# Kernel optimization log

Measured on AMD Instinct MI355X. Metric: run time of the kernel, lower is better.

## Reference

```python
import jax, jax.numpy as jnp
import numpy as np

HID = 1024
HEADS = 16
DH = HID // HEADS
SCALE = DH ** -0.5
L, B = 2048, 2


def setup_inputs() -> dict:
    key = jax.random.key(0)
    ks = jax.random.split(key, 16)
    inp = {
        "query": jax.random.normal(ks[0], (L, B, HID), jnp.float32),
        "key": jax.random.normal(ks[1], (L, B, HID), jnp.float32),
        "value": jax.random.normal(ks[2], (L, B, HID), jnp.float32),
        "mask": jax.random.randint(ks[3], (B, L), 0, 2).astype(bool),
    }
    # xavier-uniform linear weights (torch Linear stores [out, in]; y = x @ W.T + b)
    lim = (6.0 / (HID + HID)) ** 0.5
    for i, name in enumerate(["wq", "wk", "wv", "wfc"]):
        inp[name] = jax.random.uniform(ks[4 + i], (HID, HID), jnp.float32, -lim, lim)
    inp["bq"] = jnp.zeros((HID,), jnp.float32)
    inp["bk"] = jnp.zeros((HID,), jnp.float32)
    inp["bv"] = jnp.zeros((HID,), jnp.float32)
    inp["bfc"] = jnp.zeros((HID,), jnp.float32)
    inp["tao"] = jnp.full((HEADS,), 10.0, jnp.float32)
    return inp


def reference(query, key, value, mask, wq, bq, wk, bk, wv, bv, wfc, bfc, tao):
    # inputs arrive [L, B, D]; module transposes to [B, L, D]
    q = jnp.swapaxes(query, 0, 1)
    k = jnp.swapaxes(key, 0, 1)
    v = jnp.swapaxes(value, 0, 1)
    bsz, length, _ = q.shape

    def heads(x, w, b):
        y = x @ w.T + b                      # [B, L, D]
        return y.reshape(bsz, length, HEADS, DH).transpose(0, 2, 1, 3)  # [B, H, L, d]

    Q = heads(q, wq, bq)
    K = heads(k, wk, bk)
    V = heads(v, wv, bv)

    qk = jnp.einsum("bhqd,bhkd->bhqk", Q, K) * SCALE  # [B, H, L, L]

    # gaussian positional bias: -|i-j|^2/2 * tao_h^-4
    idx = jnp.arange(length, dtype=jnp.float32)
    dist = -0.5 * (idx[:, None] - idx[None, :]) ** 2          # [L, L]
    qk = qk + dist[None, None, :, :] * (tao ** -4)[None, :, None, None]

    qk = jnp.where(mask[:, None, None, :], -jnp.inf, qk)
    attn = jax.nn.softmax(qk, axis=-1)  # dropout is identity in eval mode

    x = jnp.einsum("bhqk,bhkd->bhqd", attn, V)            # [B, H, L, d]
    x = x.transpose(0, 2, 1, 3).reshape(bsz, length, HID)  # [B, L, D]
    x = x @ wfc.T + bfc
    return jnp.swapaxes(x, 0, 1)  # [L, B, D]
```

## Files before the change

kernel.cpp:

```cpp
#include <hip/hip_runtime.h>

#define LQ   2048
#define BQ   2
#define HID  1024
#define NH   16
#define DH   64
#define SCALE 0.125f
#define L2E  1.44269504088896f
#define C1   0.18033688011f
#define EXPOFF 23.0831206542f
#define MASKNEG (-1024.0f)

using short8  = __attribute__((ext_vector_type(8))) short;
using ushort8 = __attribute__((ext_vector_type(8))) unsigned short;
using f32x4   = __attribute__((ext_vector_type(4))) float;
typedef unsigned short u16;
typedef __attribute__((ext_vector_type(2))) __bf16 bf16x2;

__device__ inline u16 f2bf(float x) {
    unsigned int u = __float_as_uint(x);
    u = (u + 0x7fffu + ((u >> 16) & 1u)) >> 16;
    return (u16)u;
}

#if defined(__has_builtin)
#if __has_builtin(__builtin_amdgcn_cvt_pk_bf16_f32)
#define HAVE_PKBF 1
#endif
#if __has_builtin(__builtin_amdgcn_exp2f)
#define HAVE_EXP2 1
#endif
#endif

__device__ inline unsigned int pkbf(float a, float b) {
#ifdef HAVE_PKBF
    bf16x2 r = __builtin_amdgcn_cvt_pk_bf16_f32(a, b);
    return __builtin_bit_cast(unsigned int, r);
#else
    return (unsigned int)f2bf(a) | ((unsigned int)f2bf(b) << 16);
#endif
}

__device__ inline float fexp2(float x) {
#ifdef HAVE_EXP2
    return __builtin_amdgcn_exp2f(x);
#else
    return exp2f(x);
#endif
}

__device__ inline void gl_lds16(const void* g, void* l) {
    __builtin_amdgcn_global_load_lds(
        (const __attribute__((address_space(1))) void*)g,
        (__attribute__((address_space(3))) void*)l, 16, 0, 0);
}

struct CastArgs {
    const float* s[7];
    u16* d[7];
    int n[7];
    const unsigned char* mraw;
    float* mout;
    int mn;
};

__global__ __launch_bounds__(256) void castw(CastArgs a) {
    const int y = blockIdx.y;
    const int t = threadIdx.x;
    if (y == 7) {
        if (blockIdx.x != 0) return;
        __shared__ int cnt;
        if (t == 0) cnt = 0;
        __syncthreads();
        int local = 0;
        for (int i = t; i < a.mn; i += 256)
            if ((i & 3) && a.mraw[i]) local++;
        atomicAdd(&cnt, local);
        __syncthreads();
        bool isInt32 = (cnt == 0);
        const int* mi = (const int*)a.mraw;
        for (int i = t; i < a.mn; i += 256) {
            const bool m = isInt32 ? (mi[i] != 0) : (a.mraw[i] != 0);
            a.mout[i] = m ? (MASKNEG - EXPOFF) : (-EXPOFF);
        }
        return;
    }
    const float* s = a.s[y];
    u16* d = a.d[y];
    const int n4 = a.n[y] >> 2;
    for (int i = blockIdx.x * 256 + t; i < n4; i += gridDim.x * 256) {
        float4 v = *(const float4*)(s + (size_t)i * 4);
        uint2 p;
        p.x = pkbf(v.x, v.y);
        p.y = pkbf(v.z, v.w);
        *(uint2*)(d + (size_t)i * 4) = p;
    }
}

struct QkvArgs {
    const u16* A[3];
    const u16* W[3];
    const float* bias[3];
    u16* out[3];
};

__global__ __launch_bounds__(256) void gemm_qkv(QkvArgs ga) {
    __shared__ u16 As[2][128][64];
    __shared__ u16 Bs[2][128][64];

    const int z = blockIdx.z;
    const u16* A = ga.A[z];
    const u16* W = ga.W[z];
    const float* bias = ga.bias[z];
    u16* outp = ga.out[z];

    const int t = threadIdx.x;
    const int m0 = blockIdx.x * 128;
    const int n0 = blockIdx.y * 128;
    const int lane = t & 63;
    const int lane15 = lane & 15;
    const int quad = lane >> 4;
    const int w = t >> 6;
    const int wm = (w >> 1) * 64;
    const int wn = (w & 1) * 64;

    const int lrow = lane >> 3;
    const int ch = (lane & 7) ^ ((lane >> 3) & 7);
    const u16* aS = A + (size_t)(m0 + 32 * w + lrow) * HID + 8 * ch;
    const u16* bS = W + (size_t)(n0 + 32 * w + lrow) * HID + 8 * ch;

    const int s0 = (quad ^ (lane15 & 7)) * 8;
    const int s1 = ((4 + quad) ^ (lane15 & 7)) * 8;

    f32x4 acc[4][4];
#pragma unroll
    for (int i = 0; i < 4; i++)
#pragma unroll
        for (int j = 0; j < 4; j++) acc[i][j] = (f32x4){0,0,0,0};

#pragma unroll
    for (int i = 0; i < 4; i++) {
        gl_lds16(aS + (size_t)(8 * i) * HID, &As[0][32 * w + 8 * i][0]);
        gl_lds16(bS + (size_t)(8 * i) * HID, &Bs[0][32 * w + 8 * i][0]);
    }
    __syncthreads();

    int p = 0;
    for (int k0 = 0; k0 < HID; k0 += 64) {
        short8 af0[4], af1[4], bf0[4], bf1[4];
#pragma unroll
        for (int i = 0; i < 4; i++) {
            const u16* ar = &As[p][wm + i * 16 + lane15][0];
            const u16* br = &Bs[p][wn + i * 16 + lane15][0];
            af0[i] = *(const short8*)(ar + s0);
            af1[i] = *(const short8*)(ar + s1);
            bf0[i] = *(const short8*)(br + s0);
            bf1[i] = *(const short8*)(br + s1);
        }
        if (k0 + 64 < HID) {
#pragma unroll
            for (int i = 0; i < 4; i++) {
                gl_lds16(aS + (size_t)(8 * i) * HID + (k0 + 64), &As[p ^ 1][32 * w + 8 * i][0]);
                gl_lds16(bS + (size_t)(8 * i) * HID + (k0 + 64), &Bs[p ^ 1][32 * w + 8 * i][0]);
            }
        }
#pragma unroll
        for (int mi = 0; mi < 4; mi++)
#pragma unroll
            for (int ni = 0; ni < 4; ni++) {
                acc[mi][ni] = __builtin_amdgcn_mfma_f32_16x16x32_bf16(af0[mi], bf0[ni], acc[mi][ni], 0, 0, 0);
                acc[mi][ni] = __builtin_amdgcn_mfma_f32_16x16x32_bf16(af1[mi], bf1[ni], acc[mi][ni], 0, 0, 0);
            }
        __syncthreads();
        p ^= 1;
    }

#pragma unroll
    for (int mi = 0; mi < 4; mi++) {
#pragma unroll
        for (int ni = 0; ni < 4; ni++) {
            const int n = n0 + wn + ni * 16 + lane15;
            const float bv = bias[n];
            const int h = n >> 6, d = n & 63;
#pragma unroll
            for (int r = 0; r < 4; r++) {
                const int m = m0 + wm + mi * 16 + quad * 4 + r;
                const float c = acc[mi][ni][r] + bv;
                const int b = m & 1, l = m >> 1;
                if (z < 2) {
                    outp[(((size_t)(b * NH + h)) * LQ + l) * DH + d] = f2bf(c);
                } else {
                    outp[(((size_t)(b * NH + h)) * DH + d) * LQ + l] = f2bf(c);
                }
            }
        }
    }
}

__global__ __launch_bounds__(256) void gemm_fc(const u16* __restrict__ A,
                                               const u16* __restrict__ W,
                                               const float* __restrict__ bias,
                                               float* __restrict__ outp) {
    __shared__ u16 As[2][128][64];
    __shared__ u16 Bs[2][64][64];

    const int t = threadIdx.x;
    const int m0 = blockIdx.x * 128;
    const int n0 = blockIdx.y * 64;
    const int lane = t & 63;
    const int lane15 = lane & 15;
    const int quad = lane >> 4;
    const int w = t >> 6;
    const int wm = (w >> 1) * 64;
    const int wn = (w & 1) * 32;

    const int lrow = lane >> 3;
    const int ch = (lane & 7) ^ ((lane >> 3) & 7);
    const u16* aS = A + (size_t)(m0 + 32 * w + lrow) * HID + 8 * ch;
    const u16* bS = W + (size_t)(n0 + 16 * w + lrow) * HID + 8 * ch;

    const int s0 = (quad ^ (lane15 & 7)) * 8;
    const int s1 = ((4 + quad) ^ (lane15 & 7)) * 8;

    f32x4 acc[4][2];
#pragma unroll
    for (int i = 0; i < 4; i++)
#pragma unroll
        for (int j = 0; j < 2; j++) acc[i][j] = (f32x4){0,0,0,0};

#pragma unroll
    for (int i = 0; i < 4; i++)
        gl_lds16(aS + (size_t)(8 * i) * HID, &As[0][32 * w + 8 * i][0]);
#pragma unroll
    for (int i = 0; i < 2; i++)
        gl_lds16(bS + (size_t)(8 * i) * HID, &Bs[0][16 * w + 8 * i][0]);
    __syncthreads();

    int p = 0;
    for (int k0 = 0; k0 < HID; k0 += 64) {
        short8 af0[4], af1[4], bf0[2], bf1[2];
#pragma unroll
        for (int i = 0; i < 4; i++) {
            const u16* ar = &As[p][wm + i * 16 + lane15][0];
            af0[i] = *(const short8*)(ar + s0);
            af1[i] = *(const short8*)(ar + s1);
        }
#pragma unroll
        for (int j = 0; j < 2; j++) {
            const u16* br = &Bs[p][wn + j * 16 + lane15][0];
            bf0[j] = *(const short8*)(br + s0);
            bf1[j] = *(const short8*)(br + s1);
        }
        if (k0 + 64 < HID) {
#pragma unroll
            for (int i = 0; i < 4; i++)
                gl_lds16(aS + (size_t)(8 * i) * HID + (k0 + 64), &As[p ^ 1][32 * w + 8 * i][0]);
#pragma unroll
            for (int i = 0; i < 2; i++)
                gl_lds16(bS + (size_t)(8 * i) * HID + (k0 + 64), &Bs[p ^ 1][16 * w + 8 * i][0]);
        }
#pragma unroll
        for (int mi = 0; mi < 4; mi++)
#pragma unroll
            for (int ni = 0; ni < 2; ni++) {
                acc[mi][ni] = __builtin_amdgcn_mfma_f32_16x16x32_bf16(af0[mi], bf0[ni], acc[mi][ni], 0, 0, 0);
                acc[mi][ni] = __builtin_amdgcn_mfma_f32_16x16x32_bf16(af1[mi], bf1[ni], acc[mi][ni], 0, 0, 0);
            }
        __syncthreads();
        p ^= 1;
    }

#pragma unroll
    for (int mi = 0; mi < 4; mi++) {
#pragma unroll
        for (int ni = 0; ni < 2; ni++) {
            const int n = n0 + wn + ni * 16 + lane15;
            const float bv = bias[n];
#pragma unroll
            for (int r = 0; r < 4; r++) {
                const int m = m0 + wm + mi * 16 + quad * 4 + r;
                outp[(size_t)m * HID + n] = acc[mi][ni][r] + bv;
            }
        }
    }
}

#define PSTR 72

__global__ __launch_bounds__(256, 3) void attn_kernel(const u16* __restrict__ Qg,
                                                      const u16* __restrict__ Kg,
                                                      const u16* __restrict__ Vtg,
                                                      const float* __restrict__ maskF,
                                                      const float* __restrict__ tao,
                                                      u16* __restrict__ Xa) {
    __shared__ u16 Ks[2][64][64];
    __shared__ u16 Vt[2][64][64];
    __shared__ u16 PT[64][PSTR];

    const int bh = blockIdx.x;
    const int q0 = blockIdx.y * 64;
    const int b = bh >> 4;
    const int h = bh & 15;
    const int t = threadIdx.x;
    const int w = t >> 6;
    const int lane = t & 63;
    const int lane15 = lane & 15;
    const int quad = lane >> 4;

    const u16* Kbase = Kg + (size_t)bh * LQ * DH;
    const u16* Vtbase = Vtg + (size_t)bh * DH * LQ;
    const float* mrow = maskF + b * LQ;

    const float tv = tao[h];
    const float t2 = tv * tv;
    const float nb = -0.5f / (t2 * t2);
    const float nb2 = nb * L2E;
    const float sqn = sqrtf(-nb2);
    const float R = sqrtf(-40.0f / nb2) + 1.0f;

    int c_lo = (int)floorf(((float)q0 - R) * (1.0f / 64.0f));
    int c_hi = (int)floorf(((float)(q0 + 63) + R) * (1.0f / 64.0f));
    if (c_lo < 0) c_lo = 0;
    if (c_hi > (LQ / 64 - 1)) c_hi = LQ / 64 - 1;
    if (c_hi < c_lo) c_hi = c_lo;

    const int lr = lane >> 3;
    const int sch = (lane & 7) ^ lr;
    const u16* kS0 = Kbase + (size_t)(16 * w + lr) * DH + 8 * sch;
    const u16* kS1 = Kbase + (size_t)(16 * w + 8 + lr) * DH + 8 * sch;
    const u16* vS0 = Vtbase + (size_t)(16 * w + lr) * LQ + 8 * sch;
    const u16* vS1 = Vtbase + (size_t)(16 * w + 8 + lr) * LQ + 8 * sch;

    const int qrow = q0 + w * 16 + lane15;
    short8 qB0, qB1;
    {
        const u16* qp_ = Qg + ((size_t)bh * LQ + qrow) * DH + quad * 8;
        qB0 = *(const short8*)(qp_);
        qB1 = *(const short8*)(qp_ + 32);
    }

    const int s0 = (quad ^ (lane15 & 7)) * 8;
    const int s1 = ((4 + quad) ^ (lane15 & 7)) * 8;

    float crs[16];
#pragma unroll
    for (int i = 0; i < 16; i++)
        crs[i] = (float)((i >> 2) * 16 + (i & 3)) * sqn;

    short8 ones;
#pragma unroll
    for (int i = 0; i < 8; i++) ones[i] = (short)0x3F80;

    f32x4 O[4];
#pragma unroll
    for (int mt = 0; mt < 4; mt++) O[mt] = (f32x4){0,0,0,0};
    f32x4 Lacc = (f32x4){0,0,0,0};

    const float eb0 = (float)(qrow - quad * 4);
    const int prow = w * 16 + lane15;

    gl_lds16(kS0 + (size_t)c_lo * (64 * DH), &Ks[0][16 * w][0]);
    gl_lds16(kS1 + (size_t)c_lo * (64 * DH), &Ks[0][16 * w + 8][0]);
    gl_lds16(vS0 + 64 * c_lo, &Vt[0][16 * w][0]);
    gl_lds16(vS1 + 64 * c_lo, &Vt[0][16 * w + 8][0]);
    __syncthreads();

    int p = 0;
    for (int c = c_lo; c <= c_hi; ++c) {
        float4 mv[4];
#pragma unroll
        for (int kt = 0; kt < 4; kt++)
            mv[kt] = *(const float4*)(mrow + 64 * c + kt * 16 + quad * 4);

        if (c < c_hi) {
            gl_lds16(kS0 + (size_t)(c + 1) * (64 * DH), &Ks[p ^ 1][16 * w][0]);
            gl_lds16(kS1 + (size_t)(c + 1) * (64 * DH), &Ks[p ^ 1][16 * w + 8][0]);
            gl_lds16(vS0 + 64 * (c + 1), &Vt[p ^ 1][16 * w][0]);
            gl_lds16(vS1 + 64 * (c + 1), &Vt[p ^ 1][16 * w + 8][0]);
        }

        f32x4 S[4];
#pragma unroll
        for (int kt = 0; kt < 4; kt++) {
            const u16* kr = &Ks[p][kt * 16 + lane15][0];
            const short8 ka = *(const short8*)(kr + s0);
            const short8 kb = *(const short8*)(kr + s1);
            S[kt] = __builtin_amdgcn_mfma_f32_16x16x32_bf16(ka, qB0, (f32x4){0,0,0,0}, 0, 0, 0);
            S[kt] = __builtin_amdgcn_mfma_f32_16x16x32_bf16(kb, qB1, S[kt], 0, 0, 0);
        }

        const float ebS = (eb0 - (float)(64 * c)) * sqn;
        float lacc_dummy;
        (void)lacc_dummy;
#pragma unroll
        for (int kt = 0; kt < 4; kt++) {
            float pr[4];
#pragma unroll
            for (int r = 0; r < 4; r++) {
                const float dp = ebS - crs[kt * 4 + r];
                const float tb = fmaf(-dp, dp, ((const float*)&mv[kt])[r]);
                pr[r] = fexp2(fmaf(S[kt][r], C1, tb));
            }
            uint2 pk2;
            pk2.x = pkbf(pr[0], pr[1]);
            pk2.y = pkbf(pr[2], pr[3]);
            *(uint2*)&PT[prow][kt * 16 + quad * 4] = pk2;
        }

        const short8 pB0 = *(const short8*)&PT[prow][quad * 8];
        const short8 pB1 = *(const short8*)&PT[prow][32 + quad * 8];
        Lacc = __builtin_amdgcn_mfma_f32_16x16x32_bf16(ones, pB0, Lacc, 0, 0, 0);
        Lacc = __builtin_amdgcn_mfma_f32_16x16x32_bf16(ones, pB1, Lacc, 0, 0, 0);
#pragma unroll
        for (int mt = 0; mt < 4; mt++) {
            const u16* vr = &Vt[p][mt * 16 + lane15][0];
            const short8 va = *(const short8*)(vr + s0);
            const short8 vb = *(const short8*)(vr + s1);
            O[mt] = __builtin_amdgcn_mfma_f32_16x16x32_bf16(va, pB0, O[mt], 0, 0, 0);
            O[mt] = __builtin_amdgcn_mfma_f32_16x16x32_bf16(vb, pB1, O[mt], 0, 0, 0);
        }

        __syncthreads();
        p ^= 1;
    }

    {
        const float inv = 1.0f / Lacc[0];
        u16* dst = Xa + ((size_t)qrow * BQ + b) * HID + h * DH;
#pragma unroll
        for (int mt = 0; mt < 4; mt++) {
            uint2 pk2;
            pk2.x = pkbf(O[mt][0] * inv, O[mt][1] * inv);
            pk2.y = pkbf(O[mt][2] * inv, O[mt][3] * inv);
            *(uint2*)(dst + mt * 16 + quad * 4) = pk2;
        }
    }
}

extern "C" void kernel_launch(void* const* d_in, const int* in_sizes, int n_in,
                              void* d_out, int out_size, void* d_ws, size_t ws_size,
                              hipStream_t stream) {
    const float* q    = (const float*)d_in[0];
    const float* k    = (const float*)d_in[1];
    const float* v    = (const float*)d_in[2];
    const void*  mask = d_in[3];
    const float* wq   = (const float*)d_in[4];
    const float* wk   = (const float*)d_in[5];
    const float* wv   = (const float*)d_in[6];
    const float* wfc  = (const float*)d_in[7];
    const float* bq   = (const float*)d_in[8];
    const float* bk   = (const float*)d_in[9];
    const float* bv   = (const float*)d_in[10];
    const float* bfc  = (const float*)d_in[11];
    const float* tao  = (const float*)d_in[12];

    const size_t NE = (size_t)LQ * BQ * HID;
    const size_t NW = (size_t)HID * HID;
    u16* base = (u16*)d_ws;
    u16* Qp    = base;
    u16* Kp    = base + NE;
    u16* Vtp   = base + 2 * NE;
    u16* Xa    = base + 3 * NE;
    u16* qbf   = base + 4 * NE;
    u16* kbf   = base + 5 * NE;
    u16* vbf   = base + 6 * NE;
    u16* wqbf  = base + 7 * NE;
    u16* wkbf  = wqbf + NW;
    u16* wvbf  = wkbf + NW;
    u16* wfcbf = wvbf + NW;
    float* maskF = (float*)(wfcbf + NW);

    CastArgs ca;
    ca.s[0] = q;   ca.d[0] = qbf;   ca.n[0] = (int)NE;
    ca.s[1] = k;   ca.d[1] = kbf;   ca.n[1] = (int)NE;
    ca.s[2] = v;   ca.d[2] = vbf;   ca.n[2] = (int)NE;
    ca.s[3] = wq;  ca.d[3] = wqbf;  ca.n[3] = (int)NW;
    ca.s[4] = wk;  ca.d[4] = wkbf;  ca.n[4] = (int)NW;
    ca.s[5] = wv;  ca.d[5] = wvbf;  ca.n[5] = (int)NW;
    ca.s[6] = wfc; ca.d[6] = wfcbf; ca.n[6] = (int)NW;
    ca.mraw = (const unsigned char*)mask;
    ca.mout = maskF;
    ca.mn = BQ * LQ;
    castw<<<dim3(256, 8), 256, 0, stream>>>(ca);

    QkvArgs ga;
    ga.A[0] = qbf;  ga.W[0] = wqbf;  ga.bias[0] = bq;  ga.out[0] = Qp;
    ga.A[1] = kbf;  ga.W[1] = wkbf;  ga.bias[1] = bk;  ga.out[1] = Kp;
    ga.A[2] = vbf;  ga.W[2] = wvbf;  ga.bias[2] = bv;  ga.out[2] = Vtp;
    gemm_qkv<<<dim3(32, 8, 3), 256, 0, stream>>>(ga);

    attn_kernel<<<dim3(32, 32), 256, 0, stream>>>(Qp, Kp, Vtp, maskF, tao, Xa);

    gemm_fc<<<dim3(32, 16), 256, 0, stream>>>(Xa, wfcbf, bfc, (float*)d_out);
}
```

Before: 236.5 us.

## Process 128 query rows per attention block to reuse K/V tiles twice

Each attention block now covers 128 query rows instead of 64, with every wave handling two 16-row query subtiles that share the same K and V tiles in LDS. This halves the number of blocks and the K/V global-to-LDS traffic per query row, and each LDS fragment read feeds twice as many MFMAs. The cost is more accumulator registers per wave (launch bounds lowered from 3 to 2 waves per SIMD), only 512 blocks in the grid, and a slightly wider key window per block.

```diff
diff --git a/kernel.cpp b/kernel.cpp
--- a/kernel.cpp
+++ b/kernel.cpp
@@ -287,7 +287,7 @@
 
 #define PSTR 72
 
-__global__ __launch_bounds__(256, 3) void attn_kernel(const u16* __restrict__ Qg,
+__global__ __launch_bounds__(256, 2) void attn_kernel(const u16* __restrict__ Qg,
                                                       const u16* __restrict__ Kg,
                                                       const u16* __restrict__ Vtg,
                                                       const float* __restrict__ maskF,
@@ -295,10 +295,10 @@
                                                       u16* __restrict__ Xa) {
     __shared__ u16 Ks[2][64][64];
     __shared__ u16 Vt[2][64][64];
-    __shared__ u16 PT[64][PSTR];
+    __shared__ u16 PT[128][PSTR];
 
     const int bh = blockIdx.x;
-    const int q0 = blockIdx.y * 64;
+    const int q0 = blockIdx.y * 128;
     const int b = bh >> 4;
     const int h = bh & 15;
     const int t = threadIdx.x;
@@ -319,7 +319,7 @@
     const float R = sqrtf(-40.0f / nb2) + 1.0f;
 
     int c_lo = (int)floorf(((float)q0 - R) * (1.0f / 64.0f));
-    int c_hi = (int)floorf(((float)(q0 + 63) + R) * (1.0f / 64.0f));
+    int c_hi = (int)floorf(((float)(q0 + 127) + R) * (1.0f / 64.0f));
     if (c_lo < 0) c_lo = 0;
     if (c_hi > (LQ / 64 - 1)) c_hi = LQ / 64 - 1;
     if (c_hi < c_lo) c_hi = c_lo;
@@ -331,12 +331,16 @@
     const u16* vS0 = Vtbase + (size_t)(16 * w + lr) * LQ + 8 * sch;
     const u16* vS1 = Vtbase + (size_t)(16 * w + 8 + lr) * LQ + 8 * sch;
 
-    const int qrow = q0 + w * 16 + lane15;
-    short8 qB0, qB1;
+    const int qrow0 = q0 + w * 32 + lane15;
+    const int qrow1 = qrow0 + 16;
+    short8 qA00, qA01, qA10, qA11;
     {
-        const u16* qp_ = Qg + ((size_t)bh * LQ + qrow) * DH + quad * 8;
-        qB0 = *(const short8*)(qp_);
-        qB1 = *(const short8*)(qp_ + 32);
+        const u16* qp0 = Qg + ((size_t)bh * LQ + qrow0) * DH + quad * 8;
+        qA00 = *(const short8*)(qp0);
+        qA01 = *(const short8*)(qp0 + 32);
+        const u16* qp1 = Qg + ((size_t)bh * LQ + qrow1) * DH + quad * 8;
+        qA10 = *(const short8*)(qp1);
+        qA11 = *(const short8*)(qp1 + 32);
     }
 
     const int s0 = (quad ^ (lane15 & 7)) * 8;
@@ -351,13 +355,16 @@
 #pragma unroll
     for (int i = 0; i < 8; i++) ones[i] = (short)0x3F80;
 
-    f32x4 O[4];
-#pragma unroll
-    for (int mt = 0; mt < 4; mt++) O[mt] = (f32x4){0,0,0,0};
-    f32x4 Lacc = (f32x4){0,0,0,0};
-
-    const float eb0 = (float)(qrow - quad * 4);
-    const int prow = w * 16 + lane15;
+    f32x4 O0[4], O1[4];
+#pragma unroll
+    for (int mt = 0; mt < 4; mt++) { O0[mt] = (f32x4){0,0,0,0}; O1[mt] = (f32x4){0,0,0,0}; }
+    f32x4 Lac0 = (f32x4){0,0,0,0};
+    f32x4 Lac1 = (f32x4){0,0,0,0};
+
+    const float eb00 = (float)(qrow0 - quad * 4);
+    const float eb01 = (float)(qrow1 - quad * 4);
+    const int prow0 = w * 32 + lane15;
+    const int prow1 = prow0 + 16;
 
     gl_lds16(kS0 + (size_t)c_lo * (64 * DH), &Ks[0][16 * w][0]);
     gl_lds16(kS1 + (size_t)c_lo * (64 * DH), &Ks[0][16 * w + 8][0]);
@@ -379,45 +386,58 @@
             gl_lds16(vS1 + 64 * (c + 1), &Vt[p ^ 1][16 * w + 8][0]);
         }
 
-        f32x4 S[4];
+        f32x4 S0[4], S1[4];
 #pragma unroll
         for (int kt = 0; kt < 4; kt++) {
             const u16* kr = &Ks[p][kt * 16 + lane15][0];
             const short8 ka = *(const short8*)(kr + s0);
             const short8 kb = *(const short8*)(kr + s1);
-            S[kt] = __builtin_amdgcn_mfma_f32_16x16x32_bf16(ka, qB0, (f32x4){0,0,0,0}, 0, 0, 0);
-            S[kt] = __builtin_amdgcn_mfma_f32_16x16x32_bf16(kb, qB1, S[kt], 0, 0, 0);
-        }
-
-        const float ebS = (eb0 - (float)(64 * c)) * sqn;
-        float lacc_dummy;
-        (void)lacc_dummy;
+            S0[kt] = __builtin_amdgcn_mfma_f32_16x16x32_bf16(ka, qA00, (f32x4){0,0,0,0}, 0, 0, 0);
+            S0[kt] = __builtin_amdgcn_mfma_f32_16x16x32_bf16(kb, qA01, S0[kt], 0, 0, 0);
+            S1[kt] = __builtin_amdgcn_mfma_f32_16x16x32_bf16(ka, qA10, (f32x4){0,0,0,0}, 0, 0, 0);
+            S1[kt] = __builtin_amdgcn_mfma_f32_16x16x32_bf16(kb, qA11, S1[kt], 0, 0, 0);
+        }
+
+        const float ebS0 = (eb00 - (float)(64 * c)) * sqn;
+        const float ebS1 = (eb01 - (float)(64 * c)) * sqn;
 #pragma unroll
         for (int kt = 0; kt < 4; kt++) {
-            float pr[4];
+            float pr0[4], pr1[4];
 #pragma unroll
             for (int r = 0; r < 4; r++) {
-                const float dp = ebS - crs[kt * 4 + r];
-                const float tb = fmaf(-dp, dp, ((const float*)&mv[kt])[r]);
-                pr[r] = fexp2(fmaf(S[kt][r], C1, tb));
+                const float mb = ((const float*)&mv[kt])[r];
+                const float dp0 = ebS0 - crs[kt * 4 + r];
+                const float dp1 = ebS1 - crs[kt * 4 + r];
+                pr0[r] = fexp2(fmaf(S0[kt][r], C1, fmaf(-dp0, dp0, mb)));
+                pr1[r] = fexp2(fmaf(S1[kt][r], C1, fmaf(-dp1, dp1, mb)));
             }
-            uint2 pk2;
-            pk2.x = pkbf(pr[0], pr[1]);
-            pk2.y = pkbf(pr[2], pr[3]);
-            *(uint2*)&PT[prow][kt * 16 + quad * 4] = pk2;
-        }
-
-        const short8 pB0 = *(const short8*)&PT[prow][quad * 8];
-        const short8 pB1 = *(const short8*)&PT[prow][32 + quad * 8];
-        Lacc = __builtin_amdgcn_mfma_f32_16x16x32_bf16(ones, pB0, Lacc, 0, 0, 0);
-        Lacc = __builtin_amdgcn_mfma_f32_16x16x32_bf16(ones, pB1, Lacc, 0, 0, 0);
+            uint2 pk0, pk1;
+            pk0.x = pkbf(pr0[0], pr0[1]);
+            pk0.y = pkbf(pr0[2], pr0[3]);
+            pk1.x = pkbf(pr1[0], pr1[1]);
+            pk1.y = pkbf(pr1[2], pr1[3]);
+            *(uint2*)&PT[prow0][kt * 16 + quad * 4] = pk0;
+            *(uint2*)&PT[prow1][kt * 16 + quad * 4] = pk1;
+        }
+
+        const short8 pB00 = *(const short8*)&PT[prow0][quad * 8];
+        const short8 pB01 = *(const short8*)&PT[prow0][32 + quad * 8];
+        const short8 pB10 = *(const short8*)&PT[prow1][quad * 8];
+        const short8 pB11 = *(const short8*)&PT[prow1][32 + quad * 8];
+        Lac0 = __builtin_amdgcn_mfma_f32_16x16x32_bf16(ones, pB00, Lac0, 0, 0, 0);
+        Lac0 = __builtin_amdgcn_mfma_f32_16x16x32_bf16(ones, pB01, Lac0, 0, 0, 0);
+        Lac1 = __builtin_amdgcn_mfma_f32_16x16x32_bf16(ones, pB10, Lac1, 0, 0, 0);
+        Lac1 = __builtin_amdgcn_mfma_f32_16x16x32_bf16(ones, pB11, Lac1, 0, 0, 0);
+
 #pragma unroll
         for (int mt = 0; mt < 4; mt++) {
             const u16* vr = &Vt[p][mt * 16 + lane15][0];
             const short8 va = *(const short8*)(vr + s0);
             const short8 vb = *(const short8*)(vr + s1);
-            O[mt] = __builtin_amdgcn_mfma_f32_16x16x32_bf16(va, pB0, O[mt], 0, 0, 0);
-            O[mt] = __builtin_amdgcn_mfma_f32_16x16x32_bf16(vb, pB1, O[mt], 0, 0, 0);
+            O0[mt] = __builtin_amdgcn_mfma_f32_16x16x32_bf16(va, pB00, O0[mt], 0, 0, 0);
+            O0[mt] = __builtin_amdgcn_mfma_f32_16x16x32_bf16(vb, pB01, O0[mt], 0, 0, 0);
+            O1[mt] = __builtin_amdgcn_mfma_f32_16x16x32_bf16(va, pB10, O1[mt], 0, 0, 0);
+            O1[mt] = __builtin_amdgcn_mfma_f32_16x16x32_bf16(vb, pB11, O1[mt], 0, 0, 0);
         }
 
         __syncthreads();
@@ -425,14 +445,23 @@
     }
 
     {
-        const float inv = 1.0f / Lacc[0];
-        u16* dst = Xa + ((size_t)qrow * BQ + b) * HID + h * DH;
+        const float inv0 = 1.0f / Lac0[0];
+        u16* dst0 = Xa + ((size_t)qrow0 * BQ + b) * HID + h * DH;
 #pragma unroll
         for (int mt = 0; mt < 4; mt++) {
             uint2 pk2;
-            pk2.x = pkbf(O[mt][0] * inv, O[mt][1] * inv);
-            pk2.y = pkbf(O[mt][2] * inv, O[mt][3] * inv);
-            *(uint2*)(dst + mt * 16 + quad * 4) = pk2;
+            pk2.x = pkbf(O0[mt][0] * inv0, O0[mt][1] * inv0);
+            pk2.y = pkbf(O0[mt][2] * inv0, O0[mt][3] * inv0);
+            *(uint2*)(dst0 + mt * 16 + quad * 4) = pk2;
+        }
+        const float inv1 = 1.0f / Lac1[0];
+        u16* dst1 = Xa + ((size_t)qrow1 * BQ + b) * HID + h * DH;
+#pragma unroll
+        for (int mt = 0; mt < 4; mt++) {
+            uint2 pk2;
+            pk2.x = pkbf(O1[mt][0] * inv1, O1[mt][1] * inv1);
+            pk2.y = pkbf(O1[mt][2] * inv1, O1[mt][3] * inv1);
+            *(uint2*)(dst1 + mt * 16 + quad * 4) = pk2;
         }
     }
 }
@@ -489,7 +518,7 @@
     ga.A[2] = vbf;  ga.W[2] = wvbf;  ga.bias[2] = bv;  ga.out[2] = Vtp;
     gemm_qkv<<<dim3(32, 8, 3), 256, 0, stream>>>(ga);
 
-    attn_kernel<<<dim3(32, 32), 256, 0, stream>>>(Qp, Kp, Vtp, maskF, tao, Xa);
+    attn_kernel<<<dim3(32, 16), 256, 0, stream>>>(Qp, Kp, Vtp, maskF, tao, Xa);
 
     gemm_fc<<<dim3(32, 16), 256, 0, stream>>>(Xa, wfcbf, bfc, (float*)d_out);
 }
```

Result: faster. 231.5 us (-2.1%).
